# Kernel optimization log

Measured on AMD Instinct MI355X. Metric: run time of the kernel, lower is better.

Reference implementation:

```python
import jax, jax.numpy as jnp
import numpy as np

HIDDEN = 1024
HEADS = 16
HEAD_DIM = HIDDEN // HEADS


def setup_inputs() -> dict:
    key = jax.random.key(0)
    ks = jax.random.split(key, 9)
    s = 1.0 / np.sqrt(HIDDEN)  # nn.Linear default init scale (uniform bound)
    def lin(kw, kb):
        W = jax.random.uniform(kw, (HIDDEN, HIDDEN), jnp.float32, -s, s)
        b = jax.random.uniform(kb, (HIDDEN,), jnp.float32, -s, s)
        return W, b
    Wq, bq = lin(ks[0], ks[1])
    Wk, bk = lin(ks[2], ks[3])
    Wv, bv = lin(ks[4], ks[5])
    Wo, bo = lin(ks[6], ks[7])
    x = jax.random.normal(ks[8], (2, 2048, HIDDEN), jnp.float32)
    return {"x": x, "Wq": Wq, "bq": bq, "Wk": Wk, "bk": bk,
            "Wv": Wv, "bv": bv, "Wo": Wo, "bo": bo}


def reference(x, Wq, bq, Wk, bk, Wv, bv, Wo, bo):
    B, S, _ = x.shape
    # projections (torch Linear: y = x @ W.T + b)
    def proj(W, b):
        y = jnp.einsum('bsh,oh->bso', x, W) + b
        return y.reshape(B, S, HEADS, HEAD_DIM)
    q = proj(Wq, bq)  # [B,S,H,D]
    k = proj(Wk, bk)
    v = proj(Wv, bv)
    scale = 1.0 / np.sqrt(HEAD_DIM)
    scores = jnp.einsum('bqhd,bkhd->bhqk', q, k) * scale  # [B,H,S,S]
    probs = jax.nn.softmax(scores, axis=-1)
    out = jnp.einsum('bhqk,bkhd->bqhd', probs, v).reshape(B, S, HIDDEN)
    return jnp.einsum('bsh,oh->bso', out, Wo) + bo
```

## Files before the change

### kernel.cpp

```cpp
#include <hip/hip_runtime.h>
#include <hip/hip_bf16.h>
#include <stdint.h>

#define HIDDEN 1024
#define SEQ 2048
#define BATCH 2
#define HEADS 16
#define HDIM 64
#define M_TOK (BATCH * SEQ)

using bf16_t = __bf16;
typedef __attribute__((ext_vector_type(8))) __bf16 bf16x8;
typedef __attribute__((ext_vector_type(4))) float f32x4;

__device__ __forceinline__ bf16_t tobf(float f) {
  uint32_t u = __builtin_bit_cast(uint32_t, f);
  u += 0x7FFFu + ((u >> 16) & 1u);
  uint16_t h = (uint16_t)(u >> 16);
  return __builtin_bit_cast(bf16_t, h);
}

__device__ __forceinline__ void async_cp16(const bf16_t* g, bf16_t* l) {
  __builtin_amdgcn_global_load_lds(
      (const __attribute__((address_space(1))) uint32_t*)g,
      (__attribute__((address_space(3))) uint32_t*)l, 16, 0, 0);
}

__global__ __launch_bounds__(256) void k_convert(const float* __restrict__ src,
                                                 bf16_t* __restrict__ dst, int n) {
  int i = (blockIdx.x * 256 + threadIdx.x) * 4;
  if (i >= n) return;
  float4 v = *(const float4*)(src + i);
  union { bf16_t b[4]; uint64_t u; } o;
  o.b[0] = tobf(v.x); o.b[1] = tobf(v.y); o.b[2] = tobf(v.z); o.b[3] = tobf(v.w);
  *(uint64_t*)(dst + i) = o.u;
}

__global__ __launch_bounds__(256) void k_convert4(
    const float* __restrict__ s0, const float* __restrict__ s1,
    const float* __restrict__ s2, const float* __restrict__ s3,
    bf16_t* __restrict__ d0, bf16_t* __restrict__ d1,
    bf16_t* __restrict__ d2, bf16_t* __restrict__ d3) {
  const int wsel = blockIdx.y;
  const float* src = (wsel == 0) ? s0 : (wsel == 1) ? s1 : (wsel == 2) ? s2 : s3;
  bf16_t* dst = (wsel == 0) ? d0 : (wsel == 1) ? d1 : (wsel == 2) ? d2 : d3;
  int i = (blockIdx.x * 256 + threadIdx.x) * 4;
  float4 v = *(const float4*)(src + i);
  union { bf16_t b[4]; uint64_t u; } o;
  o.b[0] = tobf(v.x); o.b[1] = tobf(v.y); o.b[2] = tobf(v.z); o.b[3] = tobf(v.w);
  *(uint64_t*)(dst + i) = o.u;
}

template <int MODE>
__device__ __forceinline__ void gemm_bt_body(const bf16_t* __restrict__ A,
                                             const bf16_t* __restrict__ Bw,
                                             const float* __restrict__ bias,
                                             void* __restrict__ dst,
                                             bf16_t* As, bf16_t* Bs) {
  constexpr int K = HIDDEN;
  const int tid = threadIdx.x;
  const int lane = tid & 63;
  const int w = tid >> 6;
  const int wr = w >> 1, wc = w & 1;
  const int lr = lane & 15, lg = lane >> 4;
  const int m0 = blockIdx.x * 128;
  const int n0 = blockIdx.y * 128;

  f32x4 acc[4][4];
#pragma unroll
  for (int i = 0; i < 4; ++i)
#pragma unroll
    for (int j = 0; j < 4; ++j) acc[i][j] = f32x4{0.f, 0.f, 0.f, 0.f};

  for (int k0 = 0; k0 < K; k0 += 32) {
#pragma unroll
    for (int i = 0; i < 2; ++i) {
      int c = w * 128 + i * 64 + lane;
      int row = c >> 2, kc = c & 3;
      async_cp16(A + (size_t)(m0 + row) * K + k0 + kc * 8, As + c * 8);
      async_cp16(Bw + (size_t)(n0 + row) * K + k0 + kc * 8, Bs + c * 8);
    }
    __syncthreads();
    bf16x8 af[4], bfr[4];
#pragma unroll
    for (int mi = 0; mi < 4; ++mi)
      af[mi] = *(const bf16x8*)(As + (wr * 64 + mi * 16 + lr) * 32 + lg * 8);
#pragma unroll
    for (int ni = 0; ni < 4; ++ni)
      bfr[ni] = *(const bf16x8*)(Bs + (wc * 64 + ni * 16 + lr) * 32 + lg * 8);
#pragma unroll
    for (int mi = 0; mi < 4; ++mi)
#pragma unroll
      for (int ni = 0; ni < 4; ++ni)
        acc[mi][ni] = __builtin_amdgcn_mfma_f32_16x16x32_bf16(af[mi], bfr[ni], acc[mi][ni], 0, 0, 0);
    __syncthreads();
  }

#pragma unroll
  for (int ni = 0; ni < 4; ++ni) {
    int col = n0 + wc * 64 + ni * 16 + lr;
    float bv = bias[col];
#pragma unroll
    for (int mi = 0; mi < 4; ++mi) {
#pragma unroll
      for (int r = 0; r < 4; ++r) {
        int m = m0 + wr * 64 + mi * 16 + lg * 4 + r;
        float v = acc[mi][ni][r] + bv;
        if (MODE == 0) {
          int b = m >> 11, s = m & (SEQ - 1);
          int h = col >> 6, d = col & 63;
          ((bf16_t*)dst)[(((size_t)(b * HEADS + h) * SEQ) + s) * HDIM + d] = tobf(v);
        } else {
          ((float*)dst)[(size_t)m * HIDDEN + col] = v;
        }
      }
    }
  }
}

__global__ __launch_bounds__(256) void k_gemm_qkv(
    const bf16_t* __restrict__ A,
    const bf16_t* __restrict__ Wqb, const bf16_t* __restrict__ Wkb,
    const bf16_t* __restrict__ Wvb,
    const float* __restrict__ bq, const float* __restrict__ bk,
    const float* __restrict__ bv,
    bf16_t* __restrict__ Qb, bf16_t* __restrict__ Kb, bf16_t* __restrict__ Vb) {
  __shared__ bf16_t As[128 * 32];
  __shared__ bf16_t Bs[128 * 32];
  const int z = blockIdx.z;
  const bf16_t* Bw = (z == 0) ? Wqb : (z == 1) ? Wkb : Wvb;
  const float* bias = (z == 0) ? bq : (z == 1) ? bk : bv;
  bf16_t* dst = (z == 0) ? Qb : (z == 1) ? Kb : Vb;
  gemm_bt_body<0>(A, Bw, bias, dst, As, Bs);
}

__global__ __launch_bounds__(256) void k_gemm_out(const bf16_t* __restrict__ A,
                                                  const bf16_t* __restrict__ Bw,
                                                  const float* __restrict__ bias,
                                                  float* __restrict__ dst) {
  __shared__ bf16_t As[128 * 32];
  __shared__ bf16_t Bs[128 * 32];
  gemm_bt_body<1>(A, Bw, bias, dst, As, Bs);
}

__global__ __launch_bounds__(256) void k_attn(const bf16_t* __restrict__ Q,
                                              const bf16_t* __restrict__ Kk,
                                              const bf16_t* __restrict__ V,
                                              bf16_t* __restrict__ AO) {
  __shared__ bf16_t Vt[64 * 64];
  __shared__ bf16_t Pl[4][16 * 64];
  const int tid = threadIdx.x;
  const int lane = tid & 63;
  const int w = tid >> 6;
  const int lr = lane & 15, lg = lane >> 4;
  const int bh = blockIdx.y;
  const int q0 = blockIdx.x * 64 + w * 16;
  const bf16_t* Qh = Q + (size_t)bh * SEQ * HDIM;
  const bf16_t* Kh = Kk + (size_t)bh * SEQ * HDIM;
  const bf16_t* Vh = V + (size_t)bh * SEQ * HDIM;

  const float qscale = 0.125f * 1.44269504088896f;
  bf16x8 aq[2];
#pragma unroll
  for (int dc = 0; dc < 2; ++dc) {
    bf16x8 t = *(const bf16x8*)(Qh + (size_t)(q0 + lr) * HDIM + dc * 32 + lg * 8);
#pragma unroll
    for (int j = 0; j < 8; ++j) t[j] = tobf((float)t[j] * qscale);
    aq[dc] = t;
  }

  bf16x8 vone;
#pragma unroll
  for (int j = 0; j < 8; ++j) vone[j] = tobf(1.0f);

  float mrow[4];
  f32x4 acc[4];
  f32x4 accd = f32x4{0.f, 0.f, 0.f, 0.f};
#pragma unroll
  for (int r = 0; r < 4; ++r) mrow[r] = -1e30f;
#pragma unroll
  for (int fc = 0; fc < 4; ++fc) acc[fc] = f32x4{0.f, 0.f, 0.f, 0.f};

  for (int kt = 0; kt < SEQ / 64; ++kt) {
    const int kr0 = kt * 64;
    __syncthreads();
    {
      int k = tid >> 2, d0 = (tid & 3) * 16;
      const bf16_t* vp = Vh + (size_t)(kr0 + k) * HDIM + d0;
#pragma unroll
      for (int half = 0; half < 2; ++half) {
        bf16x8 vv = *(const bf16x8*)(vp + half * 8);
#pragma unroll
        for (int j = 0; j < 8; ++j) {
          int d = d0 + half * 8 + j;
          Vt[d * 64 + (((k >> 3) ^ (d & 7)) * 8) + (k & 7)] = vv[j];
        }
      }
    }
    __syncthreads();

    f32x4 sf[4];
    __builtin_amdgcn_s_setprio(1);
#pragma unroll
    for (int fc = 0; fc < 4; ++fc) {
      f32x4 a = f32x4{0.f, 0.f, 0.f, 0.f};
      int kr = kr0 + fc * 16 + lr;
#pragma unroll
      for (int dc = 0; dc < 2; ++dc) {
        bf16x8 bk = *(const bf16x8*)(Kh + (size_t)kr * HDIM + dc * 32 + lg * 8);
        a = __builtin_amdgcn_mfma_f32_16x16x32_bf16(aq[dc], bk, a, 0, 0, 0);
      }
      sf[fc] = a;
    }
    __builtin_amdgcn_s_setprio(0);

    float pmax[4];
#pragma unroll
    for (int r = 0; r < 4; ++r)
      pmax[r] = fmaxf(fmaxf(sf[0][r], sf[1][r]), fmaxf(sf[2][r], sf[3][r]));
    int ok = (pmax[0] <= mrow[0] + 8.f) && (pmax[1] <= mrow[1] + 8.f) &&
             (pmax[2] <= mrow[2] + 8.f) && (pmax[3] <= mrow[3] + 8.f);
    if (!__all(ok)) {
#pragma unroll
      for (int r = 0; r < 4; ++r) {
        float mx = pmax[r];
        mx = fmaxf(mx, __shfl_xor(mx, 1));
        mx = fmaxf(mx, __shfl_xor(mx, 2));
        mx = fmaxf(mx, __shfl_xor(mx, 4));
        mx = fmaxf(mx, __shfl_xor(mx, 8));
        float mn = fmaxf(mrow[r], mx);
        float sc = exp2f(mrow[r] - mn);
        mrow[r] = mn;
        accd[r] *= sc;
#pragma unroll
        for (int fc = 0; fc < 4; ++fc) acc[fc][r] *= sc;
      }
    }
    float pv[4][4];
#pragma unroll
    for (int r = 0; r < 4; ++r)
#pragma unroll
      for (int fc = 0; fc < 4; ++fc) pv[fc][r] = exp2f(sf[fc][r] - mrow[r]);

#pragma unroll
    for (int fc = 0; fc < 4; ++fc) {
      int col = fc * 16 + lr;
#pragma unroll
      for (int r = 0; r < 4; ++r) {
        int row = lg * 4 + r;
        Pl[w][row * 64 + (((col >> 3) ^ (row & 7)) * 8) + (col & 7)] = tobf(pv[fc][r]);
      }
    }

    bf16x8 pa[2];
#pragma unroll
    for (int kc = 0; kc < 2; ++kc) {
      int swz = (kc * 4 + lg) ^ (lr & 7);
      pa[kc] = *(const bf16x8*)(&Pl[w][lr * 64 + swz * 8]);
    }
    __builtin_amdgcn_s_setprio(1);
#pragma unroll
    for (int fc = 0; fc < 4; ++fc) {
      int d = fc * 16 + lr;
#pragma unroll
      for (int kc = 0; kc < 2; ++kc) {
        int swz = (kc * 4 + lg) ^ (d & 7);
        bf16x8 bv = *(const bf16x8*)(&Vt[d * 64 + swz * 8]);
        acc[fc] = __builtin_amdgcn_mfma_f32_16x16x32_bf16(pa[kc], bv, acc[fc], 0, 0, 0);
      }
    }
    accd = __builtin_amdgcn_mfma_f32_16x16x32_bf16(pa[0], vone, accd, 0, 0, 0);
    accd = __builtin_amdgcn_mfma_f32_16x16x32_bf16(pa[1], vone, accd, 0, 0, 0);
    __builtin_amdgcn_s_setprio(0);
  }

  const int b = bh >> 4, h = bh & 15;
#pragma unroll
  for (int fc = 0; fc < 4; ++fc) {
#pragma unroll
    for (int r = 0; r < 4; ++r) {
      int srow = q0 + lg * 4 + r;
      float o = acc[fc][r] / accd[r];
      AO[((size_t)(b * SEQ + srow)) * HIDDEN + h * HDIM + fc * 16 + lr] = tobf(o);
    }
  }
}

extern "C" void kernel_launch(void* const* d_in, const int* in_sizes, int n_in,
                              void* d_out, int out_size, void* d_ws, size_t ws_size,
                              hipStream_t stream) {
  const float* x  = (const float*)d_in[0];
  const float* Wq = (const float*)d_in[1];
  const float* bq = (const float*)d_in[2];
  const float* Wk = (const float*)d_in[3];
  const float* bk = (const float*)d_in[4];
  const float* Wv = (const float*)d_in[5];
  const float* bv = (const float*)d_in[6];
  const float* Wo = (const float*)d_in[7];
  const float* bo = (const float*)d_in[8];

  char* ws = (char*)d_ws;
  const size_t XB = (size_t)M_TOK * HIDDEN * 2;
  const size_t WB = (size_t)HIDDEN * HIDDEN * 2;
  bf16_t* xb  = (bf16_t*)(ws);
  bf16_t* Wqb = (bf16_t*)(ws + XB);
  bf16_t* Wkb = (bf16_t*)(ws + XB + 1 * WB);
  bf16_t* Wvb = (bf16_t*)(ws + XB + 2 * WB);
  bf16_t* Wob = (bf16_t*)(ws + XB + 3 * WB);
  bf16_t* Qb  = (bf16_t*)(ws + XB + 4 * WB);
  bf16_t* Kb  = (bf16_t*)(ws + 2 * XB + 4 * WB);
  bf16_t* Vb  = (bf16_t*)(ws + 3 * XB + 4 * WB);
  bf16_t* AOb = (bf16_t*)(ws + 4 * XB + 4 * WB);

  k_convert<<<(M_TOK * HIDDEN) / 1024, 256, 0, stream>>>(x, xb, M_TOK * HIDDEN);
  k_convert4<<<dim3((HIDDEN * HIDDEN) / 1024, 4), 256, 0, stream>>>(
      Wq, Wk, Wv, Wo, Wqb, Wkb, Wvb, Wob);

  dim3 gg(M_TOK / 128, HIDDEN / 128);
  k_gemm_qkv<<<dim3(M_TOK / 128, HIDDEN / 128, 3), 256, 0, stream>>>(
      xb, Wqb, Wkb, Wvb, bq, bk, bv, Qb, Kb, Vb);

  k_attn<<<dim3(SEQ / 64, BATCH * HEADS), 256, 0, stream>>>(Qb, Kb, Vb, AOb);

  k_gemm_out<<<gg, 256, 0, stream>>>(AOb, Wob, bo, (float*)d_out);
}
```

Before: 196.1 us.

## Double-buffer V tiles with async LDS loads and transpose-read via ds_read_tr

Replaces the per-tile synchronous V load with scalar transposed LDS stores by an async global-to-LDS copy into a double buffer, prefetching the next tile while the current one is processed. V operands for the PV MFMA are then read with the hardware transposing LDS read (ds_read_b64_tr_b16), so no manual transpose is needed. This removes one barrier per iteration and the scalar scatter stores, and it overlaps the V fetch with compute. In exchange it relies on exact lane-to-address mapping for the transpose read, and there is no explicit wait on the async copy before the barrier, which risks a race.

```diff
diff --git a/kernel.cpp b/kernel.cpp
--- a/kernel.cpp
+++ b/kernel.cpp
@@ -11,6 +11,7 @@
 
 using bf16_t = __bf16;
 typedef __attribute__((ext_vector_type(8))) __bf16 bf16x8;
+typedef __attribute__((ext_vector_type(4))) __bf16 bf16x4;
 typedef __attribute__((ext_vector_type(4))) float f32x4;
 
 __device__ __forceinline__ bf16_t tobf(float f) {
@@ -25,6 +26,10 @@
       (const __attribute__((address_space(1))) uint32_t*)g,
       (__attribute__((address_space(3))) uint32_t*)l, 16, 0, 0);
 }
+
+#define TRR(dst, a, IMM)                                              \
+  asm volatile("ds_read_b64_tr_b16 %0, %1 offset:" IMM                \
+               : "=v"(dst) : "v"(a))
 
 __global__ __launch_bounds__(256) void k_convert(const float* __restrict__ src,
                                                  bf16_t* __restrict__ dst, int n) {
@@ -147,7 +152,7 @@
                                               const bf16_t* __restrict__ Kk,
                                               const bf16_t* __restrict__ V,
                                               bf16_t* __restrict__ AO) {
-  __shared__ bf16_t Vt[64 * 64];
+  __shared__ __align__(16) bf16_t Vl[2][4096];
   __shared__ bf16_t Pl[4][16 * 64];
   const int tid = threadIdx.x;
   const int lane = tid & 63;
@@ -159,6 +164,14 @@
   const bf16_t* Kh = Kk + (size_t)bh * SEQ * HDIM;
   const bf16_t* Vh = V + (size_t)bh * SEQ * HDIM;
 
+  const int s_kb = lane >> 5, s_dc = (lane >> 3) & 3, s_kr = (lane >> 1) & 3,
+            s_h = lane & 1;
+  const int lane_goff = (s_kb * 4 + s_kr) * HDIM + s_dc * 16 + s_h * 8;
+
+  const uint32_t lds_v0 =
+      (uint32_t)(uintptr_t)(__attribute__((address_space(3))) bf16_t*)&Vl[0][0];
+  const uint32_t vbase = lds_v0 + (uint32_t)(1024 * lg + 8 * lr);
+
   const float qscale = 0.125f * 1.44269504088896f;
   bf16x8 aq[2];
 #pragma unroll
@@ -181,23 +194,22 @@
 #pragma unroll
   for (int fc = 0; fc < 4; ++fc) acc[fc] = f32x4{0.f, 0.f, 0.f, 0.f};
 
+  auto stage = [&](int ktile, int buf) {
+#pragma unroll
+    for (int t = 0; t < 2; ++t) {
+      int n = 2 * w + t;
+      async_cp16(Vh + (size_t)(ktile * 64 + n * 8) * HDIM + lane_goff,
+                 &Vl[buf][n * 512]);
+    }
+  };
+
+  stage(0, 0);
+
   for (int kt = 0; kt < SEQ / 64; ++kt) {
+    const int cur = kt & 1;
     const int kr0 = kt * 64;
     __syncthreads();
-    {
-      int k = tid >> 2, d0 = (tid & 3) * 16;
-      const bf16_t* vp = Vh + (size_t)(kr0 + k) * HDIM + d0;
-#pragma unroll
-      for (int half = 0; half < 2; ++half) {
-        bf16x8 vv = *(const bf16x8*)(vp + half * 8);
-#pragma unroll
-        for (int j = 0; j < 8; ++j) {
-          int d = d0 + half * 8 + j;
-          Vt[d * 64 + (((k >> 3) ^ (d & 7)) * 8) + (k & 7)] = vv[j];
-        }
-      }
-    }
-    __syncthreads();
+    if (kt + 1 < SEQ / 64) stage(kt + 1, cur ^ 1);
 
     f32x4 sf[4];
     __builtin_amdgcn_s_setprio(1);
@@ -258,17 +270,29 @@
       int swz = (kc * 4 + lg) ^ (lr & 7);
       pa[kc] = *(const bf16x8*)(&Pl[w][lr * 64 + swz * 8]);
     }
+
+    union Uf { bf16x4 h[2]; bf16x8 v; };
+    Uf vf[4][2];
+    {
+      uint32_t va = vbase + (uint32_t)(cur * 8192);
+      TRR(vf[0][0].h[0], va, "0");    TRR(vf[0][0].h[1], va, "512");
+      TRR(vf[1][0].h[0], va, "128");  TRR(vf[1][0].h[1], va, "640");
+      TRR(vf[2][0].h[0], va, "256");  TRR(vf[2][0].h[1], va, "768");
+      TRR(vf[3][0].h[0], va, "384");  TRR(vf[3][0].h[1], va, "896");
+      TRR(vf[0][1].h[0], va, "4096"); TRR(vf[0][1].h[1], va, "4608");
+      TRR(vf[1][1].h[0], va, "4224"); TRR(vf[1][1].h[1], va, "4736");
+      TRR(vf[2][1].h[0], va, "4352"); TRR(vf[2][1].h[1], va, "4864");
+      TRR(vf[3][1].h[0], va, "4480"); TRR(vf[3][1].h[1], va, "4992");
+      asm volatile("s_waitcnt lgkmcnt(0)" ::: "memory");
+      __builtin_amdgcn_sched_barrier(0);
+    }
+
     __builtin_amdgcn_s_setprio(1);
 #pragma unroll
-    for (int fc = 0; fc < 4; ++fc) {
-      int d = fc * 16 + lr;
-#pragma unroll
-      for (int kc = 0; kc < 2; ++kc) {
-        int swz = (kc * 4 + lg) ^ (d & 7);
-        bf16x8 bv = *(const bf16x8*)(&Vt[d * 64 + swz * 8]);
-        acc[fc] = __builtin_amdgcn_mfma_f32_16x16x32_bf16(pa[kc], bv, acc[fc], 0, 0, 0);
-      }
-    }
+    for (int fc = 0; fc < 4; ++fc)
+#pragma unroll
+      for (int kc = 0; kc < 2; ++kc)
+        acc[fc] = __builtin_amdgcn_mfma_f32_16x16x32_bf16(pa[kc], vf[fc][kc].v, acc[fc], 0, 0, 0);
     accd = __builtin_amdgcn_mfma_f32_16x16x32_bf16(pa[0], vone, accd, 0, 0, 0);
     accd = __builtin_amdgcn_mfma_f32_16x16x32_bf16(pa[1], vone, accd, 0, 0, 0);
     __builtin_amdgcn_s_setprio(0);
```

After: 258.4 us. 31.8% more time.

## Write V transposed from QKV GEMM and read it directly in attention

Applied to the files above, without the earlier changes.

The V projection epilogue now stores V in a [B,H,D,S] transposed layout, so the attention kernel can load MFMA B-operands for P·V straight from global memory. This removes the per-tile LDS transpose of V and the two __syncthreads per key tile. The trade-off is strided global stores in the GEMM epilogue, where consecutive lanes write addresses SEQ apart, and uncached global reads of V inside the attention inner loop instead of shared-memory reuse across the 4 waves.

```diff
diff --git a/kernel.cpp b/kernel.cpp
--- a/kernel.cpp
+++ b/kernel.cpp
@@ -110,6 +110,10 @@
           int b = m >> 11, s = m & (SEQ - 1);
           int h = col >> 6, d = col & 63;
           ((bf16_t*)dst)[(((size_t)(b * HEADS + h) * SEQ) + s) * HDIM + d] = tobf(v);
+        } else if (MODE == 2) {
+          int b = m >> 11, s = m & (SEQ - 1);
+          int h = col >> 6, d = col & 63;
+          ((bf16_t*)dst)[(((size_t)(b * HEADS + h) * HDIM) + d) * SEQ + s] = tobf(v);
         } else {
           ((float*)dst)[(size_t)m * HIDDEN + col] = v;
         }
@@ -124,14 +128,18 @@
     const bf16_t* __restrict__ Wvb,
     const float* __restrict__ bq, const float* __restrict__ bk,
     const float* __restrict__ bv,
-    bf16_t* __restrict__ Qb, bf16_t* __restrict__ Kb, bf16_t* __restrict__ Vb) {
+    bf16_t* __restrict__ Qb, bf16_t* __restrict__ Kb, bf16_t* __restrict__ VTb) {
   __shared__ bf16_t As[128 * 32];
   __shared__ bf16_t Bs[128 * 32];
   const int z = blockIdx.z;
-  const bf16_t* Bw = (z == 0) ? Wqb : (z == 1) ? Wkb : Wvb;
-  const float* bias = (z == 0) ? bq : (z == 1) ? bk : bv;
-  bf16_t* dst = (z == 0) ? Qb : (z == 1) ? Kb : Vb;
-  gemm_bt_body<0>(A, Bw, bias, dst, As, Bs);
+  if (z == 2) {
+    gemm_bt_body<2>(A, Wvb, bv, VTb, As, Bs);
+  } else {
+    const bf16_t* Bw = (z == 0) ? Wqb : Wkb;
+    const float* bias = (z == 0) ? bq : bk;
+    bf16_t* dst = (z == 0) ? Qb : Kb;
+    gemm_bt_body<0>(A, Bw, bias, dst, As, Bs);
+  }
 }
 
 __global__ __launch_bounds__(256) void k_gemm_out(const bf16_t* __restrict__ A,
@@ -145,9 +153,8 @@
 
 __global__ __launch_bounds__(256) void k_attn(const bf16_t* __restrict__ Q,
                                               const bf16_t* __restrict__ Kk,
-                                              const bf16_t* __restrict__ V,
+                                              const bf16_t* __restrict__ VT,
                                               bf16_t* __restrict__ AO) {
-  __shared__ bf16_t Vt[64 * 64];
   __shared__ bf16_t Pl[4][16 * 64];
   const int tid = threadIdx.x;
   const int lane = tid & 63;
@@ -157,7 +164,7 @@
   const int q0 = blockIdx.x * 64 + w * 16;
   const bf16_t* Qh = Q + (size_t)bh * SEQ * HDIM;
   const bf16_t* Kh = Kk + (size_t)bh * SEQ * HDIM;
-  const bf16_t* Vh = V + (size_t)bh * SEQ * HDIM;
+  const bf16_t* VhT = VT + (size_t)bh * HDIM * SEQ;
 
   const float qscale = 0.125f * 1.44269504088896f;
   bf16x8 aq[2];
@@ -183,21 +190,6 @@
 
   for (int kt = 0; kt < SEQ / 64; ++kt) {
     const int kr0 = kt * 64;
-    __syncthreads();
-    {
-      int k = tid >> 2, d0 = (tid & 3) * 16;
-      const bf16_t* vp = Vh + (size_t)(kr0 + k) * HDIM + d0;
-#pragma unroll
-      for (int half = 0; half < 2; ++half) {
-        bf16x8 vv = *(const bf16x8*)(vp + half * 8);
-#pragma unroll
-        for (int j = 0; j < 8; ++j) {
-          int d = d0 + half * 8 + j;
-          Vt[d * 64 + (((k >> 3) ^ (d & 7)) * 8) + (k & 7)] = vv[j];
-        }
-      }
-    }
-    __syncthreads();
 
     f32x4 sf[4];
     __builtin_amdgcn_s_setprio(1);
@@ -261,11 +253,10 @@
     __builtin_amdgcn_s_setprio(1);
 #pragma unroll
     for (int fc = 0; fc < 4; ++fc) {
-      int d = fc * 16 + lr;
+      const bf16_t* vrow = VhT + (size_t)(fc * 16 + lr) * SEQ + kr0;
 #pragma unroll
       for (int kc = 0; kc < 2; ++kc) {
-        int swz = (kc * 4 + lg) ^ (d & 7);
-        bf16x8 bv = *(const bf16x8*)(&Vt[d * 64 + swz * 8]);
+        bf16x8 bv = *(const bf16x8*)(vrow + kc * 32 + lg * 8);
         acc[fc] = __builtin_amdgcn_mfma_f32_16x16x32_bf16(pa[kc], bv, acc[fc], 0, 0, 0);
       }
     }
@@ -309,7 +300,7 @@
   bf16_t* Wob = (bf16_t*)(ws + XB + 3 * WB);
   bf16_t* Qb  = (bf16_t*)(ws + XB + 4 * WB);
   bf16_t* Kb  = (bf16_t*)(ws + 2 * XB + 4 * WB);
-  bf16_t* Vb  = (bf16_t*)(ws + 3 * XB + 4 * WB);
+  bf16_t* VTb = (bf16_t*)(ws + 3 * XB + 4 * WB);
   bf16_t* AOb = (bf16_t*)(ws + 4 * XB + 4 * WB);
 
   k_convert<<<(M_TOK * HIDDEN) / 1024, 256, 0, stream>>>(x, xb, M_TOK * HIDDEN);
@@ -318,9 +309,9 @@
 
   dim3 gg(M_TOK / 128, HIDDEN / 128);
   k_gemm_qkv<<<dim3(M_TOK / 128, HIDDEN / 128, 3), 256, 0, stream>>>(
-      xb, Wqb, Wkb, Wvb, bq, bk, bv, Qb, Kb, Vb);
-
-  k_attn<<<dim3(SEQ / 64, BATCH * HEADS), 256, 0, stream>>>(Qb, Kb, Vb, AOb);
+      xb, Wqb, Wkb, Wvb, bq, bk, bv, Qb, Kb, VTb);
+
+  k_attn<<<dim3(SEQ / 64, BATCH * HEADS), 256, 0, stream>>>(Qb, Kb, VTb, AOb);
 
   k_gemm_out<<<gg, 256, 0, stream>>>(AOb, Wob, bo, (float*)d_out);
 }
```

Result: slower. 318.6 us (+62.5%).
